# Performance work log

Hardware: AMD Instinct MI355X
Metric: run time of the kernel (lower is better)

## Reference

```python
import jax, jax.numpy as jnp
import numpy as np

HEADS = 8
DIM_HEAD = 128
ATTN_MATRIX_SCALE = 1.5  # tau applied to mean-centered logits
SCALE = DIM_HEAD ** -0.5


def setup_inputs() -> dict:
    key = jax.random.key(0)
    ks = jax.random.split(key, 7)
    b, n, m = 2, 2048, 2048
    qd, cd, inner = 1024, 768, HEADS * DIM_HEAD
    x = jax.random.normal(ks[0], (b, n, qd), dtype=jnp.float32)
    context = jax.random.normal(ks[1], (b, m, cd), dtype=jnp.float32)
    Wq = jax.random.normal(ks[2], (qd, inner), dtype=jnp.float32) * (qd ** -0.5)
    Wk = jax.random.normal(ks[3], (cd, inner), dtype=jnp.float32) * (cd ** -0.5)
    Wv = jax.random.normal(ks[4], (cd, inner), dtype=jnp.float32) * (cd ** -0.5)
    Wout = jax.random.normal(ks[5], (inner, qd), dtype=jnp.float32) * (inner ** -0.5)
    bout = jnp.zeros((qd,), dtype=jnp.float32)
    return {"x": x, "context": context, "Wq": Wq, "Wk": Wk, "Wv": Wv,
            "Wout": Wout, "bout": bout}


def _split_heads(t):
    # (b, n, h*d) -> (h, b*n, d); matches rearrange '(b h) n d -> h (b n) d'
    b, n, _ = t.shape
    t = t.reshape(b, n, HEADS, DIM_HEAD)
    return t.transpose(2, 0, 1, 3).reshape(HEADS, b * n, DIM_HEAD)


def reference(x, context, Wq, Wk, Wv, Wout, bout):
    b, n, _ = x.shape
    qh = _split_heads(jnp.einsum('bnq,qi->bni', x, Wq))        # (h, b*n, d)
    kh = _split_heads(jnp.einsum('bmc,ci->bmi', context, Wk))  # (h, b*m, d)
    vh = _split_heads(jnp.einsum('bmc,ci->bmi', context, Wv))  # (h, b*m, d)

    # custom mean-centered / tau-scaled similarity (_compute_sim_with_tau)
    sim = jnp.einsum('hid,hjd->hij', qh, kh) * SCALE
    mean = jnp.mean(sim, axis=-1, keepdims=True)
    sim = (sim - mean) * ATTN_MATRIX_SCALE + mean

    attn = jax.nn.softmax(sim, axis=-1)
    out = jnp.einsum('hij,hjd->hid', attn, vh)                 # (h, b*n, d)

    # (h, b*n, d) -> (b, n, h*d)
    out = out.reshape(HEADS, b, n, DIM_HEAD).transpose(1, 2, 0, 3)
    out = out.reshape(b, n, HEADS * DIM_HEAD)
    return jnp.einsum('bni,iq->bnq', out, Wout) + bout
```

## Files before the change

### kernel.cpp

```cpp
#include <hip/hip_runtime.h>
#include <cstdint>
#include <cstddef>

typedef unsigned short u16t;
typedef __bf16 bf16x8_t __attribute__((ext_vector_type(8)));
typedef float f32x4_t __attribute__((ext_vector_type(4)));

#define MFMA_BF16 __builtin_amdgcn_mfma_f32_16x16x32_bf16

__device__ __forceinline__ u16t f2bf(float f) {
    uint32_t u = __builtin_bit_cast(uint32_t, f);
    u += 0x7fffu + ((u >> 16) & 1u);
    return (u16t)(u >> 16);
}

__device__ __forceinline__ uint32_t pk2bf(float a, float b) {
    return (uint32_t)f2bf(a) | ((uint32_t)f2bf(b) << 16);
}

__device__ __forceinline__ bf16x8_t ld_frag(const u16t* p) {
    return __builtin_bit_cast(bf16x8_t, *(const uint4*)p);
}

__device__ __forceinline__ void gl_lds16(const u16t* g, u16t* l) {
    __builtin_amdgcn_global_load_lds(
        (const __attribute__((address_space(1))) void*)g,
        (__attribute__((address_space(3))) void*)l, 16, 0, 0);
}

__global__ void cast_bf16_kernel(const float* __restrict__ src, u16t* __restrict__ dst, int n4) {
    int i = blockIdx.x * blockDim.x + threadIdx.x;
    if (i >= n4) return;
    float4 v = ((const float4*)src)[i];
    uint2 o;
    o.x = pk2bf(v.x, v.y);
    o.y = pk2bf(v.z, v.w);
    ((uint2*)dst)[i] = o;
}

__global__ void transpose_cast_kernel(const float* __restrict__ W, u16t* __restrict__ Wt,
                                      int K, int N) {
    __shared__ float tile[32][33];
    int n0 = blockIdx.x * 32, k0 = blockIdx.y * 32;
    int tx = threadIdx.x, ty = threadIdx.y;
    for (int i = ty; i < 32; i += 8)
        tile[i][tx] = W[(size_t)(k0 + i) * N + n0 + tx];
    __syncthreads();
    for (int i = ty; i < 32; i += 8)
        Wt[(size_t)(n0 + i) * K + k0 + tx] = f2bf(tile[tx][i]);
}

__global__ __launch_bounds__(256) void gemm_bf16_kernel(
    const u16t* __restrict__ A, const u16t* __restrict__ Bt,
    int K, void* __restrict__ outp, const float* __restrict__ bias,
    int mode, float oscale)
{
    __shared__ __align__(16) u16t As[2][128 * 64];
    __shared__ __align__(16) u16t Bs[2][64 * 64];
    const int bm = blockIdx.y * 128, bn = blockIdx.x * 64;
    const int tid = threadIdx.x;
    const int wave = tid >> 6, lane = tid & 63;
    const int wm = wave & 1, wn = wave >> 1;
    const int quad = lane >> 4, l16 = lane & 15;

    const int l8r = lane >> 3, l8c = lane & 7;
    const int cgx = (l8c ^ l8r) * 8;

    f32x4_t acc[4][2];
#pragma unroll
    for (int i = 0; i < 4; ++i)
#pragma unroll
        for (int j = 0; j < 2; ++j) acc[i][j] = (f32x4_t){0.f, 0.f, 0.f, 0.f};

    const int nk = K >> 6;

#pragma unroll
    for (int it = 0; it < 4; ++it) {
        int rb = wave * 32 + it * 8;
        gl_lds16(&A[(size_t)(bm + rb + l8r) * K + cgx], &As[0][rb * 64]);
    }
#pragma unroll
    for (int it = 0; it < 2; ++it) {
        int rb = wave * 16 + it * 8;
        gl_lds16(&Bt[(size_t)(bn + rb + l8r) * K + cgx], &Bs[0][rb * 64]);
    }

    for (int ki = 0; ki < nk; ++ki) {
        const int buf = ki & 1;
        __syncthreads();

        if (ki + 1 < nk) {
            const int kc = (ki + 1) << 6;
#pragma unroll
            for (int it = 0; it < 4; ++it) {
                int rb = wave * 32 + it * 8;
                gl_lds16(&A[(size_t)(bm + rb + l8r) * K + kc + cgx], &As[buf ^ 1][rb * 64]);
            }
#pragma unroll
            for (int it = 0; it < 2; ++it) {
                int rb = wave * 16 + it * 8;
                gl_lds16(&Bt[(size_t)(bn + rb + l8r) * K + kc + cgx], &Bs[buf ^ 1][rb * 64]);
            }
        }

#pragma unroll
        for (int ks = 0; ks < 2; ++ks) {
            bf16x8_t af[4], bfv[2];
#pragma unroll
            for (int i = 0; i < 4; ++i) {
                int r = wm * 64 + i * 16 + l16;
                af[i] = ld_frag(&As[buf][r * 64 + (((ks * 4 + quad) ^ (r & 7)) * 8)]);
            }
#pragma unroll
            for (int j = 0; j < 2; ++j) {
                int r = wn * 32 + j * 16 + l16;
                bfv[j] = ld_frag(&Bs[buf][r * 64 + (((ks * 4 + quad) ^ (r & 7)) * 8)]);
            }
#pragma unroll
            for (int i = 0; i < 4; ++i)
#pragma unroll
                for (int j = 0; j < 2; ++j)
                    acc[i][j] = MFMA_BF16(af[i], bfv[j], acc[i][j], 0, 0, 0);
        }
    }

    if (mode == 3) {
        float* out = (float*)outp;
#pragma unroll
        for (int j = 0; j < 2; ++j) {
            int c = bn + wn * 32 + j * 16 + l16;
            float b = bias[c];
#pragma unroll
            for (int i = 0; i < 4; ++i) {
                int rb = bm + wm * 64 + i * 16 + quad * 4;
#pragma unroll
                for (int r = 0; r < 4; ++r)
                    out[(size_t)(rb + r) * 1024 + c] = acc[i][j][r] + b;
            }
        }
    } else if (mode == 2) {
        u16t* out = (u16t*)outp;
#pragma unroll
        for (int i = 0; i < 4; ++i)
#pragma unroll
            for (int j = 0; j < 2; ++j) {
                int rb = bm + wm * 64 + i * 16 + quad * 4;
                int c = bn + wn * 32 + j * 16 + l16;
                int h = c >> 7, d = c & 127;
                uint2 pk;
                pk.x = pk2bf(acc[i][j][0], acc[i][j][1]);
                pk.y = pk2bf(acc[i][j][2], acc[i][j][3]);
                *(uint2*)&out[((size_t)h * 128 + d) * 4096 + rb] = pk;
            }
    } else {
        u16t* out = (u16t*)outp;
#pragma unroll
        for (int i = 0; i < 4; ++i)
#pragma unroll
            for (int j = 0; j < 2; ++j) {
                int rb = bm + wm * 64 + i * 16 + quad * 4;
                int c = bn + wn * 32 + j * 16 + l16;
                int h = c >> 7, d = c & 127;
#pragma unroll
                for (int r = 0; r < 4; ++r)
                    out[((size_t)h * 4096 + rb + r) * 128 + d] = f2bf(acc[i][j][r] * oscale);
            }
    }
}

__global__ __launch_bounds__(256) void flash_kernel(
    const u16t* __restrict__ Qh, const u16t* __restrict__ Kh,
    const u16t* __restrict__ Vtg, u16t* __restrict__ Oh)
{
    extern __shared__ __align__(16) u16t smem[];
    u16t* Ps = smem + 32768;

    const int h = blockIdx.x;
    const int q0 = blockIdx.y * 64;
    const int tid = threadIdx.x;
    const int wave = tid >> 6, lane = tid & 63;
    const int quad = lane >> 4, l16 = lane & 15;

    const u16t* Kg = Kh + (size_t)h * 4096 * 128;
    const u16t* Vg = Vtg + (size_t)h * 128 * 4096;

    {
        const u16t* Qg = Qh + ((size_t)h * 4096 + q0) * 128;
        const int sr = tid >> 4, c8 = tid & 15;
#pragma unroll
        for (int it = 0; it < 4; ++it) {
            int r = sr + it * 16;
            uint4 v = *(const uint4*)&Qg[r * 128 + c8 * 8];
            *(uint4*)&smem[r * 128 + ((c8 ^ (r & 15)) * 8)] = v;
        }
    }
    __syncthreads();
    bf16x8_t qf[4];
    {
        int r = wave * 16 + l16;
#pragma unroll
        for (int ks = 0; ks < 4; ++ks)
            qf[ks] = ld_frag(&smem[r * 128 + (((ks * 4 + quad) ^ (r & 15)) * 8)]);
    }
    __syncthreads();

    const int rK = lane >> 4, cK = lane & 15;
    const int rV = lane >> 3, cV = lane & 7;

#pragma unroll
    for (int it = 0; it < 4; ++it) {
        int r = wave * 16 + it * 4 + rK;
        gl_lds16(Kg + (size_t)r * 128 + (cK ^ (r & 15)) * 8,
                 smem + (wave * 16 + it * 4) * 128);
        int rv = wave * 32 + it * 8 + rV;
        gl_lds16(Vg + (size_t)rv * 4096 + (cV ^ (rv & 7)) * 8,
                 smem + 16384 + (wave * 32 + it * 8) * 64);
    }

    f32x4_t O[8];
#pragma unroll
    for (int dt = 0; dt < 8; ++dt) O[dt] = (f32x4_t){0.f, 0.f, 0.f, 0.f};
    float lsum = 0.f;
    const int prow = wave * 16 + l16;

    for (int kb = 0; kb < 64; ++kb) {
        const int bo  = (kb & 1) * 8192;
        const int bon = 8192 - bo;
        __syncthreads();

        if (kb < 63) {
            const int j0n = (kb + 1) * 64;
#pragma unroll
            for (int it = 0; it < 4; ++it) {
                int r = wave * 16 + it * 4 + rK;
                gl_lds16(Kg + ((size_t)(j0n + r)) * 128 + (cK ^ (r & 15)) * 8,
                         smem + bon + (wave * 16 + it * 4) * 128);
                int rv = wave * 32 + it * 8 + rV;
                gl_lds16(Vg + (size_t)rv * 4096 + j0n + (cV ^ (rv & 7)) * 8,
                         smem + 16384 + bon + (wave * 32 + it * 8) * 64);
            }
        }

        const u16t* Ks = smem + bo;
        const u16t* Vs = smem + 16384 + bo;

        f32x4_t S[4];
#pragma unroll
        for (int jt = 0; jt < 4; ++jt) {
            S[jt] = (f32x4_t){0.f, 0.f, 0.f, 0.f};
            int rk = jt * 16 + l16;
#pragma unroll
            for (int ks = 0; ks < 4; ++ks) {
                bf16x8_t kf = ld_frag(&Ks[rk * 128 + (((ks * 4 + quad) ^ (rk & 15)) * 8)]);
                S[jt] = MFMA_BF16(kf, qf[ks], S[jt], 0, 0, 0);
            }
        }

#pragma unroll
        for (int jt = 0; jt < 4; ++jt) {
            float e0 = __builtin_amdgcn_exp2f(S[jt][0]);
            float e1 = __builtin_amdgcn_exp2f(S[jt][1]);
            float e2 = __builtin_amdgcn_exp2f(S[jt][2]);
            float e3 = __builtin_amdgcn_exp2f(S[jt][3]);
            lsum += (e0 + e1) + (e2 + e3);
            uint2 pk;
            pk.x = pk2bf(e0, e1);
            pk.y = pk2bf(e2, e3);
            int ch = (jt * 2 + (quad >> 1)) ^ (prow & 7);
            *(uint2*)&Ps[prow * 64 + ch * 8 + (quad & 1) * 4] = pk;
        }

#pragma unroll
        for (int ks2 = 0; ks2 < 2; ++ks2) {
            bf16x8_t pf = ld_frag(&Ps[prow * 64 + (((ks2 * 4 + quad) ^ (prow & 7)) * 8)]);
#pragma unroll
            for (int dt = 0; dt < 8; ++dt) {
                int rv = dt * 16 + l16;
                bf16x8_t vf = ld_frag(&Vs[rv * 64 + (((ks2 * 4 + quad) ^ (rv & 7)) * 8)]);
                O[dt] = MFMA_BF16(vf, pf, O[dt], 0, 0, 0);
            }
        }
    }

    lsum += __shfl_xor(lsum, 16, 64);
    lsum += __shfl_xor(lsum, 32, 64);
    float inv = 1.f / lsum;
    size_t i = (size_t)(q0 + wave * 16 + l16);
#pragma unroll
    for (int dt = 0; dt < 8; ++dt) {
        uint2 pk;
        pk.x = pk2bf(O[dt][0] * inv, O[dt][1] * inv);
        pk.y = pk2bf(O[dt][2] * inv, O[dt][3] * inv);
        *(uint2*)&Oh[i * 1024 + h * 128 + dt * 16 + quad * 4] = pk;
    }
}

extern "C" void kernel_launch(void* const* d_in, const int* in_sizes, int n_in,
                              void* d_out, int out_size, void* d_ws, size_t ws_size,
                              hipStream_t stream)
{
    (void)in_sizes; (void)n_in; (void)out_size; (void)ws_size;
    const float* x    = (const float*)d_in[0];
    const float* ctx  = (const float*)d_in[1];
    const float* Wq   = (const float*)d_in[2];
    const float* Wk   = (const float*)d_in[3];
    const float* Wv   = (const float*)d_in[4];
    const float* Wout = (const float*)d_in[5];
    const float* bout = (const float*)d_in[6];
    float* out = (float*)d_out;

    u16t* ws = (u16t*)d_ws;
    u16t* x_bf   = ws;
    u16t* ctx_bf = x_bf + 4194304;
    u16t* Wqt    = ctx_bf + 3145728;
    u16t* Wkt    = Wqt + 1048576;
    u16t* Wvt    = Wkt + 786432;
    u16t* Woutt  = Wvt + 786432;
    u16t* Qh     = Woutt + 1048576;
    u16t* Kh     = Qh + 4194304;
    u16t* Vt     = Kh + 4194304;
    u16t* Oh     = x_bf;

    constexpr float QSCALE = 1.5f * 0.08838834764831845f * 1.4426950408889634f;

    (void)hipFuncSetAttribute((const void*)flash_kernel,
                              hipFuncAttributeMaxDynamicSharedMemorySize, 73728);

    cast_bf16_kernel<<<4096, 256, 0, stream>>>(x, x_bf, 1048576);
    cast_bf16_kernel<<<3072, 256, 0, stream>>>(ctx, ctx_bf, 786432);
    transpose_cast_kernel<<<dim3(32, 32), dim3(32, 8), 0, stream>>>(Wq, Wqt, 1024, 1024);
    transpose_cast_kernel<<<dim3(32, 24), dim3(32, 8), 0, stream>>>(Wk, Wkt, 768, 1024);
    transpose_cast_kernel<<<dim3(32, 24), dim3(32, 8), 0, stream>>>(Wv, Wvt, 768, 1024);
    transpose_cast_kernel<<<dim3(32, 32), dim3(32, 8), 0, stream>>>(Wout, Woutt, 1024, 1024);

    gemm_bf16_kernel<<<dim3(16, 32), 256, 0, stream>>>(x_bf,   Wqt, 1024, Qh, nullptr, 0, QSCALE);
    gemm_bf16_kernel<<<dim3(16, 32), 256, 0, stream>>>(ctx_bf, Wkt,  768, Kh, nullptr, 0, 1.0f);
    gemm_bf16_kernel<<<dim3(16, 32), 256, 0, stream>>>(ctx_bf, Wvt,  768, Vt, nullptr, 2, 1.0f);

    flash_kernel<<<dim3(8, 64), 256, 73728, stream>>>(Qh, Kh, Vt, Oh);

    gemm_bf16_kernel<<<dim3(16, 32), 256, 0, stream>>>(Oh, Woutt, 1024, out, bout, 3, 1.0f);
}
```

Baseline: 275.7 us.

## Split attention over two key halves and add a partial-result combine kernel

The flash kernel now splits the 4096 keys into two halves along a new grid z dimension, doubling the number of blocks. Each block writes unnormalized bf16 partial outputs plus per-row exp sums, and a new combine kernel adds the two halves and normalizes. The key tile shrinks from 64 to 32 rows, and K and V loads are split between wave roles. That halves the LDS footprint, so more blocks fit per CU. The cost is an extra kernel launch and memory pass, more barriers per key processed, and extra bf16 rounding of the unnormalized partials.

Measured after the change: 276.2 us. About the same (+0.2%).

```diff
diff --git a/kernel.cpp b/kernel.cpp
--- a/kernel.cpp
+++ b/kernel.cpp
@@ -16,6 +16,13 @@
 
 __device__ __forceinline__ uint32_t pk2bf(float a, float b) {
     return (uint32_t)f2bf(a) | ((uint32_t)f2bf(b) << 16);
+}
+
+__device__ __forceinline__ float bflo(uint32_t u) {
+    return __builtin_bit_cast(float, u << 16);
+}
+__device__ __forceinline__ float bfhi(uint32_t u) {
+    return __builtin_bit_cast(float, u & 0xffff0000u);
 }
 
 __device__ __forceinline__ bf16x8_t ld_frag(const u16t* p) {
@@ -170,19 +177,21 @@
 
 __global__ __launch_bounds__(256) void flash_kernel(
     const u16t* __restrict__ Qh, const u16t* __restrict__ Kh,
-    const u16t* __restrict__ Vtg, u16t* __restrict__ Oh)
+    const u16t* __restrict__ Vtg, u16t* __restrict__ Op0,
+    u16t* __restrict__ Op1, float* __restrict__ lp)
 {
     extern __shared__ __align__(16) u16t smem[];
-    u16t* Ps = smem + 32768;
+    u16t* Ps = smem + 16384;
 
     const int h = blockIdx.x;
     const int q0 = blockIdx.y * 64;
+    const int z = blockIdx.z;
     const int tid = threadIdx.x;
     const int wave = tid >> 6, lane = tid & 63;
     const int quad = lane >> 4, l16 = lane & 15;
 
-    const u16t* Kg = Kh + (size_t)h * 4096 * 128;
-    const u16t* Vg = Vtg + (size_t)h * 128 * 4096;
+    const u16t* Kg = Kh + (size_t)h * 4096 * 128 + (size_t)z * 2048 * 128;
+    const u16t* Vg = Vtg + (size_t)h * 128 * 4096 + z * 2048;
 
     {
         const u16t* Qg = Qh + ((size_t)h * 4096 + q0) * 128;
@@ -205,16 +214,24 @@
     __syncthreads();
 
     const int rK = lane >> 4, cK = lane & 15;
-    const int rV = lane >> 3, cV = lane & 7;
-
-#pragma unroll
-    for (int it = 0; it < 4; ++it) {
-        int r = wave * 16 + it * 4 + rK;
-        gl_lds16(Kg + (size_t)r * 128 + (cK ^ (r & 15)) * 8,
-                 smem + (wave * 16 + it * 4) * 128);
-        int rv = wave * 32 + it * 8 + rV;
-        gl_lds16(Vg + (size_t)rv * 4096 + (cV ^ (rv & 7)) * 8,
-                 smem + 16384 + (wave * 32 + it * 8) * 64);
+    const int rV = lane >> 2, cV = lane & 3;
+    const bool kRole = wave < 2;
+    const int wh = wave & 1;
+
+    if (kRole) {
+#pragma unroll
+        for (int it = 0; it < 4; ++it) {
+            int row = wh * 16 + it * 4 + rK;
+            gl_lds16(Kg + (size_t)row * 128 + ((cK ^ (row & 15)) * 8),
+                     smem + (wh * 16 + it * 4) * 128);
+        }
+    } else {
+#pragma unroll
+        for (int it = 0; it < 4; ++it) {
+            int row = wh * 64 + it * 16 + rV;
+            gl_lds16(Vg + (size_t)row * 4096 + ((cV ^ ((row >> 1) & 3)) * 8),
+                     smem + 8192 + (wh * 64 + it * 16) * 32);
+        }
     }
 
     f32x4_t O[8];
@@ -222,31 +239,38 @@
     for (int dt = 0; dt < 8; ++dt) O[dt] = (f32x4_t){0.f, 0.f, 0.f, 0.f};
     float lsum = 0.f;
     const int prow = wave * 16 + l16;
+    const int psw = (prow >> 1) & 3;
 
     for (int kb = 0; kb < 64; ++kb) {
-        const int bo  = (kb & 1) * 8192;
-        const int bon = 8192 - bo;
+        const int bo  = (kb & 1) * 4096;
+        const int bon = 4096 - bo;
         __syncthreads();
 
         if (kb < 63) {
-            const int j0n = (kb + 1) * 64;
-#pragma unroll
-            for (int it = 0; it < 4; ++it) {
-                int r = wave * 16 + it * 4 + rK;
-                gl_lds16(Kg + ((size_t)(j0n + r)) * 128 + (cK ^ (r & 15)) * 8,
-                         smem + bon + (wave * 16 + it * 4) * 128);
-                int rv = wave * 32 + it * 8 + rV;
-                gl_lds16(Vg + (size_t)rv * 4096 + j0n + (cV ^ (rv & 7)) * 8,
-                         smem + 16384 + bon + (wave * 32 + it * 8) * 64);
+            const int j0n = (kb + 1) * 32;
+            if (kRole) {
+#pragma unroll
+                for (int it = 0; it < 4; ++it) {
+                    int row = wh * 16 + it * 4 + rK;
+                    gl_lds16(Kg + (size_t)(j0n + row) * 128 + ((cK ^ (row & 15)) * 8),
+                             smem + bon + (wh * 16 + it * 4) * 128);
+                }
+            } else {
+#pragma unroll
+                for (int it = 0; it < 4; ++it) {
+                    int row = wh * 64 + it * 16 + rV;
+                    gl_lds16(Vg + (size_t)row * 4096 + j0n + ((cV ^ ((row >> 1) & 3)) * 8),
+                             smem + 8192 + bon + (wh * 64 + it * 16) * 32);
+                }
             }
         }
 
         const u16t* Ks = smem + bo;
-        const u16t* Vs = smem + 16384 + bo;
-
-        f32x4_t S[4];
-#pragma unroll
-        for (int jt = 0; jt < 4; ++jt) {
+        const u16t* Vs = smem + 8192 + bo;
+
+        f32x4_t S[2];
+#pragma unroll
+        for (int jt = 0; jt < 2; ++jt) {
             S[jt] = (f32x4_t){0.f, 0.f, 0.f, 0.f};
             int rk = jt * 16 + l16;
 #pragma unroll
@@ -257,7 +281,7 @@
         }
 
 #pragma unroll
-        for (int jt = 0; jt < 4; ++jt) {
+        for (int jt = 0; jt < 2; ++jt) {
             float e0 = __builtin_amdgcn_exp2f(S[jt][0]);
             float e1 = __builtin_amdgcn_exp2f(S[jt][1]);
             float e2 = __builtin_amdgcn_exp2f(S[jt][2]);
@@ -266,17 +290,16 @@
             uint2 pk;
             pk.x = pk2bf(e0, e1);
             pk.y = pk2bf(e2, e3);
-            int ch = (jt * 2 + (quad >> 1)) ^ (prow & 7);
-            *(uint2*)&Ps[prow * 64 + ch * 8 + (quad & 1) * 4] = pk;
-        }
-
-#pragma unroll
-        for (int ks2 = 0; ks2 < 2; ++ks2) {
-            bf16x8_t pf = ld_frag(&Ps[prow * 64 + (((ks2 * 4 + quad) ^ (prow & 7)) * 8)]);
+            int ch = (jt * 2 + (quad >> 1)) ^ psw;
+            *(uint2*)&Ps[prow * 32 + ch * 8 + (quad & 1) * 4] = pk;
+        }
+
+        {
+            bf16x8_t pf = ld_frag(&Ps[prow * 32 + ((quad ^ psw) * 8)]);
 #pragma unroll
             for (int dt = 0; dt < 8; ++dt) {
                 int rv = dt * 16 + l16;
-                bf16x8_t vf = ld_frag(&Vs[rv * 64 + (((ks2 * 4 + quad) ^ (rv & 7)) * 8)]);
+                bf16x8_t vf = ld_frag(&Vs[rv * 32 + ((quad ^ ((rv >> 1) & 3)) * 8)]);
                 O[dt] = MFMA_BF16(vf, pf, O[dt], 0, 0, 0);
             }
         }
@@ -284,15 +307,34 @@
 
     lsum += __shfl_xor(lsum, 16, 64);
     lsum += __shfl_xor(lsum, 32, 64);
-    float inv = 1.f / lsum;
+    u16t* Op = z ? Op1 : Op0;
     size_t i = (size_t)(q0 + wave * 16 + l16);
+    if (quad == 0) lp[z * 32768 + i * 8 + h] = lsum;
 #pragma unroll
     for (int dt = 0; dt < 8; ++dt) {
         uint2 pk;
-        pk.x = pk2bf(O[dt][0] * inv, O[dt][1] * inv);
-        pk.y = pk2bf(O[dt][2] * inv, O[dt][3] * inv);
-        *(uint2*)&Oh[i * 1024 + h * 128 + dt * 16 + quad * 4] = pk;
-    }
+        pk.x = pk2bf(O[dt][0], O[dt][1]);
+        pk.y = pk2bf(O[dt][2], O[dt][3]);
+        *(uint2*)&Op[i * 1024 + h * 128 + dt * 16 + quad * 4] = pk;
+    }
+}
+
+__global__ __launch_bounds__(256) void combine_kernel(
+    const u16t* __restrict__ O0, const u16t* __restrict__ O1,
+    const float* __restrict__ lp, u16t* __restrict__ out)
+{
+    int t = blockIdx.x * blockDim.x + threadIdx.x;
+    int e = t << 3;
+    int i = e >> 10, h = (e >> 7) & 7;
+    float inv = 1.f / (lp[i * 8 + h] + lp[32768 + i * 8 + h]);
+    uint4 a = ((const uint4*)O0)[t];
+    uint4 b = ((const uint4*)O1)[t];
+    uint4 r;
+    r.x = pk2bf((bflo(a.x) + bflo(b.x)) * inv, (bfhi(a.x) + bfhi(b.x)) * inv);
+    r.y = pk2bf((bflo(a.y) + bflo(b.y)) * inv, (bfhi(a.y) + bfhi(b.y)) * inv);
+    r.z = pk2bf((bflo(a.z) + bflo(b.z)) * inv, (bfhi(a.z) + bfhi(b.z)) * inv);
+    r.w = pk2bf((bflo(a.w) + bflo(b.w)) * inv, (bfhi(a.w) + bfhi(b.w)) * inv);
+    ((uint4*)out)[t] = r;
 }
 
 extern "C" void kernel_launch(void* const* d_in, const int* in_sizes, int n_in,
@@ -319,12 +361,14 @@
     u16t* Qh     = Woutt + 1048576;
     u16t* Kh     = Qh + 4194304;
     u16t* Vt     = Kh + 4194304;
-    u16t* Oh     = x_bf;
+    u16t* Oh   = x_bf;
+    u16t* Ohp1 = ws + 4194304;
+    float* lp  = (float*)(ws + 8388608);
 
     constexpr float QSCALE = 1.5f * 0.08838834764831845f * 1.4426950408889634f;
 
     (void)hipFuncSetAttribute((const void*)flash_kernel,
-                              hipFuncAttributeMaxDynamicSharedMemorySize, 73728);
+                              hipFuncAttributeMaxDynamicSharedMemorySize, 36864);
 
     cast_bf16_kernel<<<4096, 256, 0, stream>>>(x, x_bf, 1048576);
     cast_bf16_kernel<<<3072, 256, 0, stream>>>(ctx, ctx_bf, 786432);
@@ -337,7 +381,8 @@
     gemm_bf16_kernel<<<dim3(16, 32), 256, 0, stream>>>(ctx_bf, Wkt,  768, Kh, nullptr, 0, 1.0f);
     gemm_bf16_kernel<<<dim3(16, 32), 256, 0, stream>>>(ctx_bf, Wvt,  768, Vt, nullptr, 2, 1.0f);
 
-    flash_kernel<<<dim3(8, 64), 256, 73728, stream>>>(Qh, Kh, Vt, Oh);
+    flash_kernel<<<dim3(8, 64, 2), 256, 36864, stream>>>(Qh, Kh, Vt, Oh, Ohp1, lp);
+    combine_kernel<<<4096, 256, 0, stream>>>(Oh, Ohp1, lp, Oh);
 
     gemm_bf16_kernel<<<dim3(16, 32), 256, 0, stream>>>(Oh, Woutt, 1024, out, bout, 3, 1.0f);
 }
```
